# Performance work log

Hardware: AMD Instinct MI355X
Metric: run time of the kernel (lower is better)

## Reference

```python
import jax, jax.numpy as jnp
import numpy as np

C = 128        # in_channels
HEADS = 4
B, D, H, W = 4, 16, 64, 64  # H must equal W for this module's matmul to type-check


def conv1x1(x, Wm, b):
    # 1x1x1 Conv3d == per-voxel linear over channels
    return jnp.einsum('bcdhw,oc->bodhw', x, Wm) + b[None, :, None, None, None]


def setup_inputs() -> dict:
    key = jax.random.key(0)
    ks = jax.random.split(key, 14)
    scale = 1.0 / np.sqrt(C)

    def wmat(k):
        return jax.random.normal(k, (C, C), jnp.float32) * scale

    def bvec(k):
        return jax.random.normal(k, (C,), jnp.float32) * 0.01

    return {
        'x':  jax.random.normal(ks[0], (B, C, D, H, W), jnp.float32),
        'Wq': wmat(ks[1]),  'bq': bvec(ks[2]),
        'Wk': wmat(ks[3]),  'bk': bvec(ks[4]),
        'Wv': wmat(ks[5]),  'bv': bvec(ks[6]),
        'Wa1': wmat(ks[7]), 'ba1': bvec(ks[8]),
        'Wa2': wmat(ks[9]), 'ba2': bvec(ks[10]),
        'Wf': wmat(ks[11]), 'bf': bvec(ks[12]),
    }


def reference(x, Wq, bq, Wk, bk, Wv, bv, Wa1, ba1, Wa2, ba2, Wf, bf):
    b, c, d, h, w = x.shape
    ch = c // HEADS  # channels per head

    q = conv1x1(x, Wq, bq).reshape(b, HEADS, ch, d, h, w)
    k = conv1x1(x, Wk, bk).reshape(b, HEADS, ch, d, h, w)
    v = conv1x1(x, Wv, bv).reshape(b, HEADS, ch, d, h, w)

    # attention over the last spatial axis: (W, H)^T @ (H, W) -> (W, W)
    attn = jnp.einsum('bhcdxi,bhcdxj->bhcdij', q, k)  # [b, heads, ch, d, W, W]
    attn = jax.nn.softmax(attn, axis=-1)
    # (W, W) @ (H=W, W) -> (W, W)
    out = jnp.einsum('bhcdik,bhcdkj->bhcdij', attn, v)
    out = out.reshape(b, c, d, h, w)

    # depth=1 attention layer: conv1x1 -> relu -> conv1x1
    out = conv1x1(jax.nn.relu(conv1x1(out, Wa1, ba1)), Wa2, ba2)
    out = conv1x1(out, Wf, bf)
    return out
```

## Files before the change

### kernel.cpp

```cpp
#include <hip/hip_runtime.h>


#define CCH 128
#define SPB 65536
#define NBATCH 4
#define WTAB 16384
#define TSZ  16384

typedef float f32x4 __attribute__((ext_vector_type(4)));
typedef __bf16 bf16x8 __attribute__((ext_vector_type(8)));
typedef short s16x8 __attribute__((ext_vector_type(8)));
typedef unsigned short u16x8 __attribute__((ext_vector_type(8)));
typedef unsigned short u16x4 __attribute__((ext_vector_type(4)));
typedef unsigned int u32x2 __attribute__((ext_vector_type(2)));

template <typename T>
static __device__ __forceinline__ auto mfma_try(T a, T b, f32x4 c, int)
    -> decltype(__builtin_amdgcn_mfma_f32_16x16x32_bf16(a, b, c, 0, 0, 0)) {
  return __builtin_amdgcn_mfma_f32_16x16x32_bf16(a, b, c, 0, 0, 0);
}
template <typename T>
static __device__ __forceinline__ f32x4 mfma_try(T a, T b, f32x4 c, long) {
  return __builtin_amdgcn_mfma_f32_16x16x32_bf16(
      __builtin_bit_cast(bf16x8, a), __builtin_bit_cast(bf16x8, b), c, 0, 0, 0);
}
static __device__ __forceinline__ f32x4 MFMA16(u16x8 a, u16x8 b, f32x4 c) {
  return mfma_try(__builtin_bit_cast(s16x8, a), __builtin_bit_cast(s16x8, b), c, 0);
}

static __device__ __forceinline__ unsigned short f2b(float f) {
  return __builtin_bit_cast(unsigned short, (__bf16)f);
}
static __device__ __forceinline__ unsigned int pk2(float a, float b) {
  return (unsigned int)f2b(a) | ((unsigned int)f2b(b) << 16);
}

static __device__ __forceinline__ void glds16(const unsigned short* g,
                                              unsigned short* l) {
  __builtin_amdgcn_global_load_lds(
      (const __attribute__((address_space(1))) unsigned int*)g,
      (__attribute__((address_space(3))) unsigned int*)l, 16, 0, 0);
}

static __device__ __forceinline__ void bar_lgkm() {
  asm volatile("s_waitcnt lgkmcnt(0)" ::: "memory");
  __builtin_amdgcn_sched_barrier(0);
  __builtin_amdgcn_s_barrier();
  __builtin_amdgcn_sched_barrier(0);
}
static __device__ __forceinline__ void bar_vm0() {
  asm volatile("s_waitcnt vmcnt(0)" ::: "memory");
  __builtin_amdgcn_sched_barrier(0);
  __builtin_amdgcn_s_barrier();
  __builtin_amdgcn_sched_barrier(0);
}

static __device__ __forceinline__ int swzc(int r, int c) {
  int slot = ((c >> 3) ^ (r & 7) ^ ((r >> 3) & 15)) & 15;
  return r * 128 + slot * 8 + (c & 7);
}
static __device__ __forceinline__ int widx(int r, int c) {
  return (r & 64) * 128 + swzc(r & 63, c);
}
static __device__ __forceinline__ int cbix(int o, int s) {
  int slot = ((s >> 3) ^ (o & 15)) & 15;
  return o * 128 + slot * 8 + (s & 7);
}
static __device__ __forceinline__ int swat(int w, int x) {
  int slot = ((x >> 3) ^ (w & 7) ^ ((w >> 3) & 7)) & 7;
  return w * 64 + slot * 8 + (x & 7);
}
static __device__ __forceinline__ int pix(int i, int j) {
  int slot = ((j >> 3) ^ (((i >> 2) & 3) << 1)) & 7;
  return i * 64 + slot * 8 + (j & 7);
}
static __device__ __forceinline__ int fdx(int o, int slot) {
  return o * 128 + ((slot ^ ((o & 7) << 2)) & 31) * 4;
}

__global__ __launch_bounds__(256) void prep_w_kernel(
    const float* __restrict__ Wq, const float* __restrict__ Wk,
    const float* __restrict__ Wv, const float* __restrict__ W1,
    const float* __restrict__ W2, const float* __restrict__ W3,
    unsigned short* __restrict__ out)
{
  const float* Ws[6] = {Wq, Wk, Wv, W1, W2, W3};
  const float* W = Ws[blockIdx.x];
  unsigned short* o = out + (size_t)blockIdx.x * WTAB;
  const int tid = threadIdx.x;
#pragma unroll
  for (int p = 0; p < 16; ++p) {
    const int base = p * 1024 + tid * 4;
    const int m = base >> 7;
    const int c0 = base & 127;
    f32x4 v = *(const f32x4*)&W[base];
    u16x4 u;
#pragma unroll
    for (int e = 0; e < 4; ++e) u[e] = f2b(v[e]);
    *(u16x4*)&o[widx(m, c0)] = u;
  }
}

__global__ __launch_bounds__(512, 2) void qkv_kernel(
    const float* __restrict__ X, const unsigned short* __restrict__ Wbf,
    const float* __restrict__ Bq, const float* __restrict__ Bk,
    const float* __restrict__ Bv,
    unsigned short* __restrict__ Yq, unsigned short* __restrict__ Yk,
    unsigned short* __restrict__ Yv)
{
  __shared__ unsigned short wt[3 * WTAB];
  __shared__ unsigned short xb[WTAB];
  __shared__ unsigned short cb[WTAB];

  const int tid  = threadIdx.x;
  const int wv   = tid >> 6;
  const int lane = tid & 63;
  const int lr   = lane & 15;
  const int lg   = lane >> 4;
  const int lin  = blockIdx.x;
  const int swz  = ((lin & 7) << 6) | (lin >> 3);
  const int sbase = (swz & 127) * 512;
  const size_t xoff = (size_t)(swz >> 7) * CCH * SPB;
  const int go = tid * 8;

#pragma unroll
  for (int t = 0; t < 3; ++t)
#pragma unroll
    for (int p = 0; p < 4; ++p)
      glds16(&Wbf[t * WTAB + p * 4096 + go], &wt[t * WTAB + p * 4096 + go]);

  float bq_v[8], bk_v[8], bv_v[8];
#pragma unroll
  for (int of = 0; of < 8; ++of) {
    bq_v[of] = Bq[of * 16 + lr];
    bk_v[of] = Bk[of * 16 + lr];
    bv_v[of] = Bv[of * 16 + lr];
  }

  const int c0  = (tid >> 3) * 2;
  const int sb8 = (tid & 7) * 4;
  const float* xrow = X + xoff + (size_t)c0 * SPB + sbase;
  unsigned int* xb32 = (unsigned int*)xb;

  f32x4 xr[8];
#pragma unroll
  for (int i = 0; i < 4; ++i) {
    xr[i]     = *(const f32x4*)&xrow[sb8 + 32 * i];
    xr[4 + i] = *(const f32x4*)&xrow[SPB + sb8 + 32 * i];
  }
#pragma unroll
  for (int i = 0; i < 4; ++i)
#pragma unroll
    for (int e = 0; e < 4; ++e)
      xb32[swzc(sb8 + 32 * i + e, c0) >> 1] = pk2(xr[i][e], xr[4 + i][e]);
  __syncthreads();

#pragma unroll
  for (int si = 0; si < 4; ++si) {
    const size_t yb =
        ((size_t)(swz >> 7) * 512 + (size_t)(swz & 127) * 4 + si) * TSZ;

    if (si < 3) {
      const float* xn = xrow + (si + 1) * 128;
#pragma unroll
      for (int i = 0; i < 4; ++i) {
        xr[i]     = *(const f32x4*)&xn[sb8 + 32 * i];
        xr[4 + i] = *(const f32x4*)&xn[SPB + sb8 + 32 * i];
      }
    }
    u16x8 afr[4];
#pragma unroll
    for (int ks = 0; ks < 4; ++ks)
      afr[ks] = *(const u16x8*)&xb[swzc(wv * 16 + lr, ks * 32 + lg * 8)];
    bar_lgkm();

    {
      f32x4 acc[8];
#pragma unroll
      for (int of = 0; of < 8; ++of) { f32x4 z = {0.f,0.f,0.f,0.f}; acc[of] = z; }
#pragma unroll
      for (int ks = 0; ks < 4; ++ks) {
        const int k0 = ks * 32 + lg * 8;
#pragma unroll
        for (int of = 0; of < 8; ++of)
          acc[of] = MFMA16(afr[ks], *(const u16x8*)&wt[widx(of*16+lr, k0)], acc[of]);
      }
#pragma unroll
      for (int of = 0; of < 8; ++of) {
        const float b = bq_v[of];
        u32x2 pk;
        pk.x = pk2(acc[of][0] + b, acc[of][1] + b);
        pk.y = pk2(acc[of][2] + b, acc[of][3] + b);
        *(u32x2*)&cb[cbix(of * 16 + lr, wv * 16 + lg * 4)] = pk;
      }
    }
    bar_lgkm();

    {
      f32x4 acc[8];
#pragma unroll
      for (int of = 0; of < 8; ++of) { f32x4 z = {0.f,0.f,0.f,0.f}; acc[of] = z; }
#pragma unroll
      for (int ks = 0; ks < 4; ++ks) {
        const int k0 = ks * 32 + lg * 8;
#pragma unroll
        for (int of = 0; of < 8; ++of)
          acc[of] = MFMA16(afr[ks], *(const u16x8*)&wt[WTAB + widx(of*16+lr, k0)], acc[of]);
      }
#pragma unroll
      for (int p = 0; p < 4; ++p) {
        const int row = p * 32 + (tid >> 4);
        const int sc  = (tid & 15) * 8;
        u16x8 v = *(const u16x8*)&cb[cbix(row, sc)];
        *(u16x8*)&Yq[yb + row * 128 + sc] = v;
      }
#pragma unroll
      for (int of = 0; of < 8; ++of) {
        const float b = bk_v[of];
        u32x2 pk;
        pk.x = pk2(acc[of][0] + b, acc[of][1] + b);
        pk.y = pk2(acc[of][2] + b, acc[of][3] + b);
        *(u32x2*)&xb[cbix(of * 16 + lr, wv * 16 + lg * 4)] = pk;
      }
    }
    bar_lgkm();

    {
      f32x4 acc[8];
#pragma unroll
      for (int of = 0; of < 8; ++of) { f32x4 z = {0.f,0.f,0.f,0.f}; acc[of] = z; }
#pragma unroll
      for (int ks = 0; ks < 4; ++ks) {
        const int k0 = ks * 32 + lg * 8;
#pragma unroll
        for (int of = 0; of < 8; ++of)
          acc[of] = MFMA16(afr[ks], *(const u16x8*)&wt[2*WTAB + widx(of*16+lr, k0)], acc[of]);
      }
#pragma unroll
      for (int p = 0; p < 4; ++p) {
        const int row = p * 32 + (tid >> 4);
        const int sc  = (tid & 15) * 8;
        u16x8 v = *(const u16x8*)&xb[cbix(row, sc)];
        *(u16x8*)&Yk[yb + row * 128 + sc] = v;
      }
#pragma unroll
      for (int of = 0; of < 8; ++of) {
        const float b = bv_v[of];
        u32x2 pk;
        pk.x = pk2(acc[of][0] + b, acc[of][1] + b);
        pk.y = pk2(acc[of][2] + b, acc[of][3] + b);
        *(u32x2*)&cb[cbix(of * 16 + lr, wv * 16 + lg * 4)] = pk;
      }
    }
    bar_lgkm();

#pragma unroll
    for (int p = 0; p < 4; ++p) {
      const int row = p * 32 + (tid >> 4);
      const int sc  = (tid & 15) * 8;
      u16x8 v = *(const u16x8*)&cb[cbix(row, sc)];
      *(u16x8*)&Yv[yb + row * 128 + sc] = v;
    }
    if (si < 3) {
#pragma unroll
      for (int i = 0; i < 4; ++i)
#pragma unroll
        for (int e = 0; e < 4; ++e)
          xb32[swzc(sb8 + 32 * i + e, c0) >> 1] = pk2(xr[i][e], xr[4 + i][e]);
      bar_lgkm();
    }
  }
}

__global__ __launch_bounds__(256, 4) void attn64_kernel(
    const unsigned short* __restrict__ Q,
    const unsigned short* __restrict__ K,
    const unsigned short* __restrict__ V,
    unsigned short* __restrict__ O)
{
  __shared__ unsigned short qt[4096];
  __shared__ unsigned short kt[4096];
  __shared__ unsigned short vt[4096];
  __shared__ unsigned short pbuf[4096];

  const int tid  = threadIdx.x;
  const int wv   = tid >> 6;
  const int lane = tid & 63;
  const int lr   = lane & 15;
  const int lg   = lane >> 4;
  const int bid  = blockIdx.x;
  const int bs   = ((bid & 7) << 10) | (bid >> 3);
  const int b_   = bs >> 11;
  const int c_   = (bs >> 4) & 127;
  const int d_   = bs & 15;
  const size_t tb = ((size_t)b_ * 512 + (size_t)d_ * 32) * TSZ + (size_t)c_ * 128;

  {
    const int x0 = (tid >> 3) * 2;
    const int w0 = (tid & 7) * 8;
    const size_t ga = tb + (size_t)(x0 >> 1) * TSZ + w0;
    u16x8 qa = *(const u16x8*)&Q[ga], qb = *(const u16x8*)&Q[ga + 64];
    u16x8 ka = *(const u16x8*)&K[ga], kb = *(const u16x8*)&K[ga + 64];
    u16x8 va = *(const u16x8*)&V[ga], vb = *(const u16x8*)&V[ga + 64];
    unsigned int* qt32 = (unsigned int*)qt;
    unsigned int* kt32 = (unsigned int*)kt;
    unsigned int* vt32 = (unsigned int*)vt;
#pragma unroll
    for (int e = 0; e < 8; ++e) {
      const int idx = swat(w0 + e, x0) >> 1;
      qt32[idx] = (unsigned int)qa[e] | ((unsigned int)qb[e] << 16);
      kt32[idx] = (unsigned int)ka[e] | ((unsigned int)kb[e] << 16);
      vt32[idx] = (unsigned int)va[e] | ((unsigned int)vb[e] << 16);
    }
  }
  __syncthreads();

  f32x4 sacc[4];
#pragma unroll
  for (int nf = 0; nf < 4; ++nf) { f32x4 z = {0.f, 0.f, 0.f, 0.f}; sacc[nf] = z; }
#pragma unroll
  for (int ks = 0; ks < 2; ++ks) {
    const int k0 = ks * 32 + lg * 8;
    u16x8 a = *(const u16x8*)&qt[swat(wv * 16 + lr, k0)];
#pragma unroll
    for (int nf = 0; nf < 4; ++nf) {
      u16x8 bb = *(const u16x8*)&kt[swat(nf * 16 + lr, k0)];
      sacc[nf] = MFMA16(a, bb, sacc[nf]);
    }
  }

#pragma unroll
  for (int r = 0; r < 4; ++r) {
    float m = fmaxf(fmaxf(sacc[0][r], sacc[1][r]), fmaxf(sacc[2][r], sacc[3][r]));
    m = fmaxf(m, __shfl_xor(m, 1));
    m = fmaxf(m, __shfl_xor(m, 2));
    m = fmaxf(m, __shfl_xor(m, 4));
    m = fmaxf(m, __shfl_xor(m, 8));
    float sum = 0.f;
#pragma unroll
    for (int nf = 0; nf < 4; ++nf) {
      float p = __expf(sacc[nf][r] - m);
      sacc[nf][r] = p;
      sum += p;
    }
    sum += __shfl_xor(sum, 1);
    sum += __shfl_xor(sum, 2);
    sum += __shfl_xor(sum, 4);
    sum += __shfl_xor(sum, 8);
    const float inv = 1.f / sum;
    const int i = wv * 16 + lg * 4 + r;
#pragma unroll
    for (int nf = 0; nf < 4; ++nf)
      pbuf[pix(i, nf * 16 + lr)] = f2b(sacc[nf][r] * inv);
  }

  f32x4 oacc[4];
#pragma unroll
  for (int nf = 0; nf < 4; ++nf) { f32x4 z = {0.f, 0.f, 0.f, 0.f}; oacc[nf] = z; }
#pragma unroll
  for (int ks = 0; ks < 2; ++ks) {
    const int k0 = ks * 32 + lg * 8;
    u16x8 a = *(const u16x8*)&pbuf[pix(wv * 16 + lr, k0)];
#pragma unroll
    for (int nf = 0; nf < 4; ++nf) {
      u16x8 bb = *(const u16x8*)&vt[swat(nf * 16 + lr, k0)];
      oacc[nf] = MFMA16(bb, a, oacc[nf]);
    }
  }

  {
    const int i = 16 * wv + lr;
    const size_t ib = tb + (size_t)(i >> 1) * TSZ + (size_t)(i & 1) * 64 + lg * 4;
#pragma unroll
    for (int nf = 0; nf < 4; ++nf) {
      u32x2 pk;
      pk.x = pk2(oacc[nf][0], oacc[nf][1]);
      pk.y = pk2(oacc[nf][2], oacc[nf][3]);
      *(u32x2*)&O[ib + nf * 16] = pk;
    }
  }
}

__global__ __launch_bounds__(256, 2) void tail_kernel(
    const unsigned short* __restrict__ Xb, const unsigned short* __restrict__ Wbf,
    const float* __restrict__ B1, const float* __restrict__ B2,
    const float* __restrict__ B3, float* __restrict__ OUT)
{
  __shared__ unsigned short wl[16384];
  __shared__ unsigned short xc[16384];
  __shared__ float bias_lds[3][128];
  float* fA = (float*)xc;

  const int tid  = threadIdx.x;
  const int wv   = tid >> 6;
  const int lane = tid & 63;
  const int lr   = lane & 15;
  const int lg   = lane >> 4;
  const int bx   = blockIdx.x;
  const int bxs  = ((bx & 7) << 6) | (bx >> 3);
  const int s0   = bxs * 128;
  const size_t xbase = (size_t)blockIdx.y * CCH * SPB;
  const size_t tbin  = ((size_t)blockIdx.y * 512 + bxs) * TSZ;
  const int go = tid * 8;

#pragma unroll
  for (int p = 0; p < 8; ++p) glds16(&Wbf[p * 2048 + go], &wl[p * 2048 + go]);

  if (tid < 128) {
    bias_lds[0][tid] = B1[tid];
    bias_lds[1][tid] = B2[tid];
    bias_lds[2][tid] = B3[tid];
  }

  {
    const int cp = tid >> 2;
    const int sq = tid & 3;
    const unsigned short* xa = Xb + tbin + (size_t)(2 * cp) * 128 + sq * 32;
    const unsigned short* xb = xa + 128;
    unsigned int* xc32 = (unsigned int*)xc;
#pragma unroll
    for (int i = 0; i < 4; ++i) {
      u16x8 a = *(const u16x8*)&xa[8 * i];
      u16x8 b = *(const u16x8*)&xb[8 * i];
#pragma unroll
      for (int e = 0; e < 8; ++e)
        xc32[swzc(sq * 32 + 8 * i + e, 2 * cp) >> 1] =
            (unsigned int)a[e] | ((unsigned int)b[e] << 16);
    }
  }
  __syncthreads();

  u16x8 bfr[2][4];
#pragma unroll
  for (int nf = 0; nf < 2; ++nf)
#pragma unroll
    for (int ks = 0; ks < 4; ++ks)
      bfr[nf][ks] = *(const u16x8*)&xc[swzc(wv * 32 + nf * 16 + lr, ks * 32 + lg * 8)];

  f32x4 acc[8][2];
  auto gemm_std = [&]() {
#pragma unroll
    for (int mf = 0; mf < 8; ++mf)
#pragma unroll
      for (int nf = 0; nf < 2; ++nf) {
        f32x4 z = {0.f, 0.f, 0.f, 0.f};
        acc[mf][nf] = z;
      }
#pragma unroll
    for (int ks = 0; ks < 4; ++ks) {
      const int k0 = ks * 32 + lg * 8;
#pragma unroll
      for (int mf = 0; mf < 8; ++mf) {
        u16x8 afr = *(const u16x8*)&wl[widx(mf * 16 + lr, k0)];
        acc[mf][0] = MFMA16(afr, bfr[0][ks], acc[mf][0]);
        acc[mf][1] = MFMA16(afr, bfr[1][ks], acc[mf][1]);
      }
    }
  };

  auto epi_chain = [&](int ci, bool relu) {
#pragma unroll
    for (int mf = 0; mf < 8; ++mf)
#pragma unroll
      for (int nf = 0; nf < 2; ++nf) {
        const int s = wv * 32 + nf * 16 + lr;
        const int cc = mf * 16 + lg * 4;
        f32x4 bb = *(const f32x4*)&bias_lds[ci][cc];
        float v0 = acc[mf][nf][0] + bb[0];
        float v1 = acc[mf][nf][1] + bb[1];
        float v2 = acc[mf][nf][2] + bb[2];
        float v3 = acc[mf][nf][3] + bb[3];
        if (relu) {
          v0 = fmaxf(v0, 0.f); v1 = fmaxf(v1, 0.f);
          v2 = fmaxf(v2, 0.f); v3 = fmaxf(v3, 0.f);
        }
        u32x2 pk;
        pk.x = pk2(v0, v1);
        pk.y = pk2(v2, v3);
        *(u32x2*)&xc[swzc(s, cc)] = pk;
      }
#pragma unroll
    for (int nf = 0; nf < 2; ++nf)
#pragma unroll
      for (int ks = 0; ks < 4; ++ks)
        bfr[nf][ks] = *(const u16x8*)&xc[swzc(wv * 32 + nf * 16 + lr, ks * 32 + lg * 8)];
  };

#pragma unroll
  for (int j = 0; j < 2; ++j) {
    gemm_std();
    bar_lgkm();
    const unsigned short* Wn = Wbf + (size_t)(j + 1) * WTAB;
#pragma unroll
    for (int p = 0; p < 8; ++p) glds16(&Wn[p * 2048 + go], &wl[p * 2048 + go]);
    epi_chain(j, j == 0);
    bar_vm0();
  }

  {
    f32x4 acc3[2][8];
#pragma unroll
    for (int sf = 0; sf < 2; ++sf)
#pragma unroll
      for (int of = 0; of < 8; ++of) {
        f32x4 z = {0.f, 0.f, 0.f, 0.f};
        acc3[sf][of] = z;
      }
#pragma unroll
    for (int ks = 0; ks < 4; ++ks) {
      const int k0 = ks * 32 + lg * 8;
#pragma unroll
      for (int of = 0; of < 8; ++of) {
        u16x8 wfr = *(const u16x8*)&wl[widx(of * 16 + lr, k0)];
        acc3[0][of] = MFMA16(bfr[0][ks], wfr, acc3[0][of]);
        acc3[1][of] = MFMA16(bfr[1][ks], wfr, acc3[1][of]);
      }
    }

#pragma unroll
    for (int half = 0; half < 2; ++half) {
#pragma unroll
      for (int sf = 0; sf < 2; ++sf)
#pragma unroll
        for (int of4 = 0; of4 < 4; ++of4) {
          const int of = half * 4 + of4;
          const int ol = of4 * 16 + lr;
          const int slot = wv * 8 + sf * 4 + lg;
          const float b = bias_lds[2][of * 16 + lr];
          f32x4 v = acc3[sf][of];
          v[0] += b; v[1] += b; v[2] += b; v[3] += b;
          *(f32x4*)&fA[fdx(ol, slot)] = v;
        }
      bar_lgkm();
#pragma unroll
      for (int p = 0; p < 8; ++p) {
        const int r  = p * 8 + (tid >> 5);
        const int cg = tid & 31;
        f32x4 v = *(const f32x4*)&fA[fdx(r, cg)];
        *(f32x4*)&OUT[xbase + (size_t)(r + half * 64) * SPB + s0 + cg * 4] = v;
      }
      if (half == 0) bar_lgkm();
    }
  }
}

extern "C" void kernel_launch(void* const* d_in, const int* in_sizes, int n_in,
                              void* d_out, int out_size, void* d_ws, size_t ws_size,
                              hipStream_t stream) {
  const float* x   = (const float*)d_in[0];
  const float* Wq  = (const float*)d_in[1];  const float* bq  = (const float*)d_in[2];
  const float* Wk  = (const float*)d_in[3];  const float* bk  = (const float*)d_in[4];
  const float* Wv  = (const float*)d_in[5];  const float* bv  = (const float*)d_in[6];
  const float* Wa1 = (const float*)d_in[7];  const float* ba1 = (const float*)d_in[8];
  const float* Wa2 = (const float*)d_in[9];  const float* ba2 = (const float*)d_in[10];
  const float* Wf  = (const float*)d_in[11]; const float* bf_ = (const float*)d_in[12];

  unsigned short* qb  = (unsigned short*)d_ws;
  unsigned short* wbf = qb + (size_t)NBATCH * CCH * SPB;
  unsigned short* kb = (unsigned short*)d_out;
  unsigned short* vb = kb + (size_t)NBATCH * CCH * SPB;

  prep_w_kernel<<<6, 256, 0, stream>>>(Wq, Wk, Wv, Wa1, Wa2, Wf, wbf);

  qkv_kernel<<<512, 512, 0, stream>>>(x, wbf, bq, bk, bv, qb, kb, vb);

  attn64_kernel<<<NBATCH * CCH * 16, 256, 0, stream>>>(qb, kb, vb, qb);

  tail_kernel<<<dim3(SPB / 128, NBATCH), 256, 0, stream>>>(
      qb, wbf + (size_t)3 * WTAB, ba1, ba2, bf_, (float*)d_out);
}
```

Measured before the change: 176.9 us.

## Hold QKV weight fragments in registers and retile waves as 2x4 spatial/output split

The QKV projection kernel now gives each wave a 64-spatial by 32-output tile instead of 16 spatial by 128 outputs. Each wave loads its slice of all three weight matrices into registers once, before the spatial loop, and reuses them across every sub-step. This removes the repeated LDS reads of weight fragments in every GEMM. The trade is much higher register pressure (24 weight fragments plus 16 activation fragments per lane), so the minimum-blocks-per-SM hint was dropped from launch bounds, which may lower occupancy.

```diff
diff --git a/kernel.cpp b/kernel.cpp
--- a/kernel.cpp
+++ b/kernel.cpp
@@ -101,7 +101,7 @@
   }
 }
 
-__global__ __launch_bounds__(512, 2) void qkv_kernel(
+__global__ __launch_bounds__(512) void qkv_kernel(
     const float* __restrict__ X, const unsigned short* __restrict__ Wbf,
     const float* __restrict__ Bq, const float* __restrict__ Bk,
     const float* __restrict__ Bv,
@@ -117,6 +117,8 @@
   const int lane = tid & 63;
   const int lr   = lane & 15;
   const int lg   = lane >> 4;
+  const int sw   = wv >> 2;
+  const int ow   = wv & 3;
   const int lin  = blockIdx.x;
   const int swz  = ((lin & 7) << 6) | (lin >> 3);
   const int sbase = (swz & 127) * 512;
@@ -129,12 +131,12 @@
     for (int p = 0; p < 4; ++p)
       glds16(&Wbf[t * WTAB + p * 4096 + go], &wt[t * WTAB + p * 4096 + go]);
 
-  float bq_v[8], bk_v[8], bv_v[8];
-#pragma unroll
-  for (int of = 0; of < 8; ++of) {
-    bq_v[of] = Bq[of * 16 + lr];
-    bk_v[of] = Bk[of * 16 + lr];
-    bv_v[of] = Bv[of * 16 + lr];
+  float bias_r[3][2];
+#pragma unroll
+  for (int of = 0; of < 2; ++of) {
+    bias_r[0][of] = Bq[ow * 32 + of * 16 + lr];
+    bias_r[1][of] = Bk[ow * 32 + of * 16 + lr];
+    bias_r[2][of] = Bv[ow * 32 + of * 16 + lr];
   }
 
   const int c0  = (tid >> 3) * 2;
@@ -155,6 +157,16 @@
       xb32[swzc(sb8 + 32 * i + e, c0) >> 1] = pk2(xr[i][e], xr[4 + i][e]);
   __syncthreads();
 
+  u16x8 wfr[3][2][4];
+#pragma unroll
+  for (int t = 0; t < 3; ++t)
+#pragma unroll
+    for (int of = 0; of < 2; ++of)
+#pragma unroll
+      for (int ks = 0; ks < 4; ++ks)
+        wfr[t][of][ks] = *(const u16x8*)
+            &wt[t * WTAB + widx(ow * 32 + of * 16 + lr, ks * 32 + lg * 8)];
+
 #pragma unroll
   for (int si = 0; si < 4; ++si) {
     const size_t yb =
@@ -168,99 +180,71 @@
         xr[4 + i] = *(const f32x4*)&xn[SPB + sb8 + 32 * i];
       }
     }
-    u16x8 afr[4];
-#pragma unroll
-    for (int ks = 0; ks < 4; ++ks)
-      afr[ks] = *(const u16x8*)&xb[swzc(wv * 16 + lr, ks * 32 + lg * 8)];
+    u16x8 afr[4][4];
+#pragma unroll
+    for (int sf = 0; sf < 4; ++sf)
+#pragma unroll
+      for (int ks = 0; ks < 4; ++ks)
+        afr[sf][ks] = *(const u16x8*)
+            &xb[swzc(sw * 64 + sf * 16 + lr, ks * 32 + lg * 8)];
     bar_lgkm();
 
-    {
-      f32x4 acc[8];
-#pragma unroll
-      for (int of = 0; of < 8; ++of) { f32x4 z = {0.f,0.f,0.f,0.f}; acc[of] = z; }
-#pragma unroll
-      for (int ks = 0; ks < 4; ++ks) {
-        const int k0 = ks * 32 + lg * 8;
-#pragma unroll
-        for (int of = 0; of < 8; ++of)
-          acc[of] = MFMA16(afr[ks], *(const u16x8*)&wt[widx(of*16+lr, k0)], acc[of]);
-      }
-#pragma unroll
-      for (int of = 0; of < 8; ++of) {
-        const float b = bq_v[of];
-        u32x2 pk;
-        pk.x = pk2(acc[of][0] + b, acc[of][1] + b);
-        pk.y = pk2(acc[of][2] + b, acc[of][3] + b);
-        *(u32x2*)&cb[cbix(of * 16 + lr, wv * 16 + lg * 4)] = pk;
-      }
-    }
-    bar_lgkm();
-
-    {
-      f32x4 acc[8];
-#pragma unroll
-      for (int of = 0; of < 8; ++of) { f32x4 z = {0.f,0.f,0.f,0.f}; acc[of] = z; }
-#pragma unroll
-      for (int ks = 0; ks < 4; ++ks) {
-        const int k0 = ks * 32 + lg * 8;
-#pragma unroll
-        for (int of = 0; of < 8; ++of)
-          acc[of] = MFMA16(afr[ks], *(const u16x8*)&wt[WTAB + widx(of*16+lr, k0)], acc[of]);
-      }
+    f32x4 acc[4][2];
+    auto gemm = [&](int t) {
+#pragma unroll
+      for (int sf = 0; sf < 4; ++sf)
+#pragma unroll
+        for (int of = 0; of < 2; ++of) {
+          f32x4 z = {0.f, 0.f, 0.f, 0.f};
+          acc[sf][of] = z;
+        }
+#pragma unroll
+      for (int ks = 0; ks < 4; ++ks)
+#pragma unroll
+        for (int sf = 0; sf < 4; ++sf)
+#pragma unroll
+          for (int of = 0; of < 2; ++of)
+            acc[sf][of] = MFMA16(afr[sf][ks], wfr[t][of][ks], acc[sf][of]);
+    };
+    auto repack = [&](int t, unsigned short* buf) {
+#pragma unroll
+      for (int sf = 0; sf < 4; ++sf)
+#pragma unroll
+        for (int of = 0; of < 2; ++of) {
+          const float b = bias_r[t][of];
+          u32x2 pk;
+          pk.x = pk2(acc[sf][of][0] + b, acc[sf][of][1] + b);
+          pk.y = pk2(acc[sf][of][2] + b, acc[sf][of][3] + b);
+          *(u32x2*)&buf[cbix(ow * 32 + of * 16 + lr,
+                             sw * 64 + sf * 16 + lg * 4)] = pk;
+        }
+    };
+    auto readback = [&](const unsigned short* buf,
+                        unsigned short* __restrict__ Y) {
 #pragma unroll
       for (int p = 0; p < 4; ++p) {
         const int row = p * 32 + (tid >> 4);
         const int sc  = (tid & 15) * 8;
-        u16x8 v = *(const u16x8*)&cb[cbix(row, sc)];
-        *(u16x8*)&Yq[yb + row * 128 + sc] = v;
-      }
-#pragma unroll
-      for (int of = 0; of < 8; ++of) {
-        const float b = bk_v[of];
-        u32x2 pk;
-        pk.x = pk2(acc[of][0] + b, acc[of][1] + b);
-        pk.y = pk2(acc[of][2] + b, acc[of][3] + b);
-        *(u32x2*)&xb[cbix(of * 16 + lr, wv * 16 + lg * 4)] = pk;
-      }
-    }
+        u16x8 v = *(const u16x8*)&buf[cbix(row, sc)];
+        *(u16x8*)&Y[yb + row * 128 + sc] = v;
+      }
+    };
+
+    gemm(0);
+    repack(0, cb);
     bar_lgkm();
 
-    {
-      f32x4 acc[8];
-#pragma unroll
-      for (int of = 0; of < 8; ++of) { f32x4 z = {0.f,0.f,0.f,0.f}; acc[of] = z; }
-#pragma unroll
-      for (int ks = 0; ks < 4; ++ks) {
-        const int k0 = ks * 32 + lg * 8;
-#pragma unroll
-        for (int of = 0; of < 8; ++of)
-          acc[of] = MFMA16(afr[ks], *(const u16x8*)&wt[2*WTAB + widx(of*16+lr, k0)], acc[of]);
-      }
-#pragma unroll
-      for (int p = 0; p < 4; ++p) {
-        const int row = p * 32 + (tid >> 4);
-        const int sc  = (tid & 15) * 8;
-        u16x8 v = *(const u16x8*)&xb[cbix(row, sc)];
-        *(u16x8*)&Yk[yb + row * 128 + sc] = v;
-      }
-#pragma unroll
-      for (int of = 0; of < 8; ++of) {
-        const float b = bv_v[of];
-        u32x2 pk;
-        pk.x = pk2(acc[of][0] + b, acc[of][1] + b);
-        pk.y = pk2(acc[of][2] + b, acc[of][3] + b);
-        *(u32x2*)&cb[cbix(of * 16 + lr, wv * 16 + lg * 4)] = pk;
-      }
-    }
+    gemm(1);
+    readback(cb, Yq);
+    repack(1, xb);
     bar_lgkm();
 
-#pragma unroll
-    for (int p = 0; p < 4; ++p) {
-      const int row = p * 32 + (tid >> 4);
-      const int sc  = (tid & 15) * 8;
-      u16x8 v = *(const u16x8*)&cb[cbix(row, sc)];
-      *(u16x8*)&Yv[yb + row * 128 + sc] = v;
-    }
+    gemm(2);
+    readback(xb, Yk);
+    repack(2, cb);
+    bar_lgkm();
+
+    readback(cb, Yv);
     if (si < 3) {
 #pragma unroll
       for (int i = 0; i < 4; ++i)
```

Measured after the change: 226.7 us. +28.1%, slower.
